# Kernel optimization log

Measured on AMD Instinct MI355X. Metric: run time of the kernel, lower is better.

The kernel has to match this reference:

```python
import jax, jax.numpy as jnp
import numpy as np

B, N, D, H = 16, 1025, 512, 8
LN_EPS = 1e-5


def _make_mask(key, n):
    # sparse adjacency over n-1 prototypes, extended with cls token (row/col 0 all ones)
    n_proto = n - 1
    adj = jax.random.bernoulli(key, 0.03, (n_proto, n_proto)).astype(jnp.float32)
    adj = jnp.clip(adj + adj.T + jnp.eye(n_proto, dtype=jnp.float32), 0.0, 1.0)
    mask = jnp.zeros((n, n), dtype=jnp.float32)
    mask = mask.at[0, :].set(1.0).at[:, 0].set(1.0)
    mask = mask.at[1:, 1:].set(adj)
    return mask


def setup_inputs() -> dict:
    key = jax.random.key(0)
    ks = jax.random.split(key, 7)
    s = 1.0 / np.sqrt(D)
    return {
        "x": jax.random.normal(ks[0], (B, N, D), dtype=jnp.float32),
        "w_qkv": jax.random.uniform(ks[1], (D, 3 * D), dtype=jnp.float32, minval=-s, maxval=s),
        "w_proj": jax.random.uniform(ks[2], (D, D), dtype=jnp.float32, minval=-s, maxval=s),
        "b_proj": jnp.zeros((D,), dtype=jnp.float32),
        "ln_gamma": jnp.ones((D,), dtype=jnp.float32),
        "ln_beta": jnp.zeros((D,), dtype=jnp.float32),
        "attn_mask": _make_mask(ks[3], N),
    }


def reference(x, w_qkv, w_proj, b_proj, ln_gamma, ln_beta, attn_mask):
    b, n, d = x.shape
    hd = d // H
    scale = hd ** -0.5
    # qkv projection: [B,N,3D] -> q,k,v each [B,H,N,hd]
    qkv = (x @ w_qkv).reshape(b, n, 3, H, hd).transpose(2, 0, 3, 1, 4)
    q, k, v = qkv[0], qkv[1], qkv[2]
    attn = jnp.einsum("bhnd,bhmd->bhnm", q, k) * scale
    attn = jnp.where(attn_mask[None, None] == 0, -jnp.inf, attn)
    attn = jax.nn.softmax(attn, axis=-1)
    o = jnp.einsum("bhnm,bhmd->bhnd", attn, v).transpose(0, 2, 1, 3).reshape(b, n, d)
    o = o @ w_proj + b_proj
    # residual: proj output + LayerNorm(proj output)
    mu = jnp.mean(o, axis=-1, keepdims=True)
    var = jnp.mean(jnp.square(o - mu), axis=-1, keepdims=True)
    ln = (o - mu) * jax.lax.rsqrt(var + LN_EPS) * ln_gamma + ln_beta
    return o + ln
```

## Files before the change

### kernel.cpp

```cpp
#include <hip/hip_runtime.h>
#include <stdint.h>

#define B_ 16
#define N_ 1025
#define D_ 512
#define H_ 8
#define HD 64
#define NP 1152
#define WM 36
#define M_ (B_*N_)
#define MP (B_*NP)
#define NTKV 17
#define NQG 72

typedef unsigned short u16;
typedef __attribute__((ext_vector_type(8))) short bf16x8;
typedef __attribute__((ext_vector_type(4))) u16 u16x4;
typedef __attribute__((ext_vector_type(8))) u16 u16x8;
typedef __attribute__((ext_vector_type(4))) float f32x4;

typedef __attribute__((address_space(1))) const uint32_t gld_t;
typedef __attribute__((address_space(3))) uint32_t lds_t;

__device__ __forceinline__ u16 f2bf(float f) {
  uint32_t u = __float_as_uint(f);
  u += 0x7FFFu + ((u >> 16) & 1u);
  return (u16)(u >> 16);
}

__device__ __forceinline__ float bf2f(u16 v) {
  return __uint_as_float(((uint32_t)v) << 16);
}

__device__ __forceinline__ uint32_t cvtpk(float a, float b) {
  uint32_t r;
  asm("v_cvt_pk_bf16_f32 %0, %1, %2" : "=v"(r) : "v"(a), "v"(b));
  return r;
}

__device__ __forceinline__ float exp2a(float x) {
  float r;
  asm("v_exp_f32 %0, %1\n\ts_nop 0" : "=v"(r) : "v"(x));
  return r;
}

__device__ __forceinline__ void gload16(const void* g, void* l) {
  __builtin_amdgcn_global_load_lds((gld_t*)g, (lds_t*)l, 16, 0, 0);
}

__global__ void k_bitmask(const float* __restrict__ mask, uint32_t* __restrict__ bm) {
  int r = blockIdx.x;
  int wave = threadIdx.x >> 6, lane = threadIdx.x & 63;
  for (int chunk = wave; chunk < 18; chunk += 4) {
    int kv = chunk * 64 + lane;
    bool pred = (r < N_) && (kv < N_) && (mask[(size_t)r * N_ + kv] != 0.0f);
    unsigned long long bal = __ballot(pred);
    if (lane == 0) {
      bm[r * WM + chunk * 2]     = (uint32_t)bal;
      bm[r * WM + chunk * 2 + 1] = (uint32_t)(bal >> 32);
    }
  }
}

__global__ __launch_bounds__(64) void k_amask(const uint32_t* __restrict__ bm, float* __restrict__ am) {
  int qg = blockIdx.x, ti = blockIdx.y;
  int lane = threadIdx.x;
  int lq = lane & 15, lg = lane >> 4;
  int q = qg * 16 + lq;
  size_t base = ((size_t)(qg * NTKV + ti) * 64 + lane) * 16;
#pragma unroll
  for (int f = 0; f < 4; ++f) {
    f32x4 o;
#pragma unroll
    for (int r = 0; r < 4; ++r) {
      int kv = ti * 64 + f * 16 + 4 * lg + r;
      uint32_t bit = (bm[q * WM + (kv >> 5)] >> (kv & 31)) & 1u;
      o[r] = bit ? 0.f : -30000.f;
    }
    *reinterpret_cast<f32x4*>(am + base + f * 4) = o;
  }
}

__global__ void k_wconv(const float* __restrict__ wqkv, const float* __restrict__ wproj,
                        u16* __restrict__ wtq, u16* __restrict__ wtp) {
  int idx = blockIdx.x * 256 + threadIdx.x;
  if (idx < 3 * D_ * D_) {
    int k = idx / (3 * D_), c = idx % (3 * D_);
    wtq[c * D_ + k] = f2bf(wqkv[idx]);
  }
  if (idx < D_ * D_) {
    int k = idx >> 9, c = idx & 511;
    wtp[c * D_ + k] = f2bf(wproj[idx]);
  }
}

__global__ void k_xconv(const float* __restrict__ x, u16* __restrict__ xb) {
  int i = blockIdx.x * 256 + threadIdx.x;
  int idx = i * 8;
  int pr = idx >> 9;
  int col = idx & 511;
  int b = pr / NP, n = pr - b * NP;
  u16x8 o;
  if (n < N_) {
    const float* src = x + ((size_t)b * N_ + n) * D_ + col;
    float4 v0 = *reinterpret_cast<const float4*>(src);
    float4 v1 = *reinterpret_cast<const float4*>(src + 4);
    o[0] = f2bf(v0.x); o[1] = f2bf(v0.y); o[2] = f2bf(v0.z); o[3] = f2bf(v0.w);
    o[4] = f2bf(v1.x); o[5] = f2bf(v1.y); o[6] = f2bf(v1.z); o[7] = f2bf(v1.w);
  } else {
    o = (u16x8){0,0,0,0,0,0,0,0};
  }
  *reinterpret_cast<u16x8*>(xb + idx) = o;
}

__global__ __launch_bounds__(256) void k_qkv(const u16* __restrict__ xb, const u16* __restrict__ wtq,
                                             u16* __restrict__ Q, u16* __restrict__ K,
                                             u16* __restrict__ Vt) {
  __shared__ u16 sA[2][128 * 64];
  __shared__ u16 sB[2][128 * 64];
  const int bid = blockIdx.x;
  const int wg = (bid & 7) * 216 + (bid >> 3);
  const int m0 = (wg / 12) * 128;
  const int n0 = (wg % 12) * 128;
  const int t = threadIdx.x;
  const int wave = t >> 6, lane = t & 63;
  const int wm = wave >> 1, wn = wave & 1;
  const int lq = lane & 15, lg = lane >> 4;

  const int srow = lane >> 3;
  const int schunk = (lane & 7) ^ srow;

  f32x4 acc[4][4] = {};

#define QSTAGE(buf, k0_)                                                          \
  {                                                                               \
    _Pragma("unroll")                                                             \
    for (int p = 0; p < 4; ++p) {                                                 \
      int row = p * 32 + wave * 8 + srow;                                         \
      gload16(xb + (size_t)(m0 + row) * 512 + (k0_) + schunk * 8,                 \
              &sA[buf][p * 2048 + wave * 512 + lane * 8]);                        \
      gload16(wtq + (size_t)(n0 + row) * 512 + (k0_) + schunk * 8,                \
              &sB[buf][p * 2048 + wave * 512 + lane * 8]);                        \
    }                                                                             \
  }

#define QCOMPUTE(buf)                                                             \
  {                                                                               \
    _Pragma("unroll")                                                             \
    for (int kk = 0; kk < 2; ++kk) {                                              \
      bf16x8 af[4], bff[4];                                                       \
      const int pc = (kk * 4 + lg) ^ (lq & 7);                                    \
      _Pragma("unroll")                                                           \
      for (int f = 0; f < 4; ++f) {                                               \
        af[f]  = *reinterpret_cast<const bf16x8*>(&sA[buf][(wm * 64 + f * 16 + lq) * 64 + pc * 8]); \
        bff[f] = *reinterpret_cast<const bf16x8*>(&sB[buf][(wn * 64 + f * 16 + lq) * 64 + pc * 8]); \
      }                                                                           \
      _Pragma("unroll")                                                           \
      for (int i = 0; i < 4; ++i)                                                 \
        _Pragma("unroll")                                                         \
        for (int j = 0; j < 4; ++j)                                               \
          acc[i][j] = __builtin_amdgcn_mfma_f32_16x16x32_bf16(af[i], bff[j], acc[i][j], 0, 0, 0); \
    }                                                                             \
  }

  QSTAGE(0, 0);
  int cur = 0;
  for (int k0 = 0; k0 < 448; k0 += 64) {
    QSTAGE(cur ^ 1, k0 + 64);
    asm volatile("s_waitcnt vmcnt(8)" ::: "memory");
    __builtin_amdgcn_s_barrier();
    QCOMPUTE(cur);
    __builtin_amdgcn_s_barrier();
    cur ^= 1;
  }
  asm volatile("s_waitcnt vmcnt(0)" ::: "memory");
  __builtin_amdgcn_s_barrier();
  QCOMPUTE(cur);
#undef QSTAGE
#undef QCOMPUTE

  if (n0 >= 1024) {
    __syncthreads();
    u16* T = (u16*)&sA[0][0];
#pragma unroll
    for (int j = 0; j < 4; ++j) {
      int c = wn * 64 + j * 16 + lq;
#pragma unroll
      for (int i = 0; i < 4; ++i) {
        int mb = wm * 64 + i * 16 + lg * 4;
        u16x4 pw;
#pragma unroll
        for (int r = 0; r < 4; ++r) pw[r] = f2bf(acc[i][j][r]);
        *reinterpret_cast<u16x4*>(&T[c * 128 + ((((mb >> 3) ^ lq) << 3) | (mb & 7))]) = pw;
      }
    }
    __syncthreads();
    int c = t & 127;
    int ch0 = (t >> 7) << 3;
    int cg = n0 + c - 1024;
    int h = cg >> 6, d = cg & 63;
    int bb = m0 / NP;
    int nb = m0 - bb * NP;
    u16* dst = Vt + (((size_t)(bb * H_ + h) * HD + d) * NP + nb);
#pragma unroll
    for (int rep = 0; rep < 8; ++rep) {
      int chunk = ch0 + rep;
      u16x8 vv = *reinterpret_cast<const u16x8*>(&T[c * 128 + ((chunk ^ (c & 15)) << 3)]);
      *reinterpret_cast<u16x8*>(&dst[chunk * 8]) = vv;
    }
  } else {
#pragma unroll
    for (int j = 0; j < 4; ++j) {
      int c = n0 + wn * 64 + j * 16 + lq;
      int which = c >> 9, h = (c >> 6) & 7, d = c & 63;
#pragma unroll
      for (int i = 0; i < 4; ++i) {
        int mbase = m0 + wm * 64 + i * 16 + lg * 4;
#pragma unroll
        for (int r = 0; r < 4; ++r) {
          int m = mbase + r;
          int b = m / NP, n = m - b * NP;
          int bh = b * H_ + h;
          float v = acc[i][j][r];
          if (which == 0) Q[((size_t)bh * NP + n) * HD + d] = f2bf(v * 0.18033688f);
          else            K[((size_t)bh * NP + n) * HD + d] = f2bf(v);
        }
      }
    }
  }
}

__global__ __launch_bounds__(512) void k_attn(const u16* __restrict__ Q, const u16* __restrict__ K,
                                              const u16* __restrict__ Vt, const float* __restrict__ am,
                                              u16* __restrict__ O) {
  __shared__ u16 sK[2][64 * 64];
  __shared__ u16 sV[2][64 * 64];
  __shared__ u16 sP[8][16 * 64];

  int bid = blockIdx.x;
  int wg = (bid & 7) * (9 * 128 / 8) + (bid >> 3);
  int bh = wg / 9, qt = wg - bh * 9;
  int b = bh >> 3, h = bh & 7;
  int t = threadIdx.x;
  int w = t >> 6, lane = t & 63;
  int lq = lane & 15, lg = lane >> 4;
  int qbase = qt * 128 + w * 16;
  int qg = qt * 8 + w;
  const u16* Qp = Q + ((size_t)bh * NP + qbase) * HD;
  const u16* Kp = K + (size_t)bh * NP * HD;
  const u16* Vp = Vt + (size_t)bh * HD * NP;
  const float* amp = am + ((size_t)qg * NTKV * 64 + lane) * 16;

  bf16x8 qf0 = *reinterpret_cast<const bf16x8*>(Qp + lq * HD + lg * 8);
  bf16x8 qf1 = *reinterpret_cast<const bf16x8*>(Qp + lq * HD + 32 + lg * 8);

  const int srow = t >> 3, sch = (t & 7) ^ (srow & 7);

  f32x4 oacc[4] = {};
  float lpart = 0.f;

#define STAGE(buf, kv0_)                                                        \
  {                                                                             \
    gload16(Kp + (size_t)((kv0_) + srow) * HD + sch * 8, &sK[buf][t * 8]);      \
    gload16(Vp + (size_t)srow * NP + (kv0_) + sch * 8,   &sV[buf][t * 8]);      \
  }

#define AML(an, ti_)                                                            \
  {                                                                             \
    const f32x4* ap = reinterpret_cast<const f32x4*>(amp + (size_t)(ti_) * 64 * 16); \
    an[0] = ap[0]; an[1] = ap[1]; an[2] = ap[2]; an[3] = ap[3];                 \
  }

#define COMPUTE(buf, ac)                                                         \
  {                                                                              \
    f32x4 s[4] = {ac[0], ac[1], ac[2], ac[3]};       \
    __builtin_amdgcn_s_setprio(1);                                               \
    _Pragma("unroll")                                                            \
    for (int kk = 0; kk < 2; ++kk) {                                             \
      bf16x8 qf = kk ? qf1 : qf0;                                                \
      int pc = (kk * 4 + lg) ^ (lq & 7);                                         \
      _Pragma("unroll")                                                          \
      for (int f = 0; f < 4; ++f) {                                              \
        bf16x8 kf = *reinterpret_cast<const bf16x8*>(&sK[buf][(f * 16 + lq) * 64 + pc * 8]); \
        s[f] = __builtin_amdgcn_mfma_f32_16x16x32_bf16(kf, qf, s[f], 0, 0, 0);   \
      }                                                                          \
    }                                                                            \
    __builtin_amdgcn_s_setprio(0);                                               \
    _Pragma("unroll")                                                            \
    for (int f = 0; f < 4; ++f) {                                                \
      _Pragma("unroll")                                                          \
      for (int r = 0; r < 4; ++r) {                                              \
        float pv = exp2a(s[f][r]);                                               \
        s[f][r] = pv;                                                            \
        lpart += pv;                                                             \
      }                                                                          \
    }                                                                            \
    _Pragma("unroll")                                                            \
    for (int f = 0; f < 4; ++f) {                                                \
      uint2 pw;                                                                  \
      pw.x = cvtpk(s[f][0], s[f][1]);                                            \
      pw.y = cvtpk(s[f][2], s[f][3]);                                            \
      int pch = (2 * f + (lg >> 1)) ^ (lq & 7);                                  \
      *reinterpret_cast<uint2*>(&sP[w][lq * 64 + pch * 8 + (lg & 1) * 4]) = pw;  \
    }                                                                            \
    __builtin_amdgcn_s_setprio(1);                                               \
    _Pragma("unroll")                                                            \
    for (int kk = 0; kk < 2; ++kk) {                                             \
      int pc = (kk * 4 + lg) ^ (lq & 7);                                         \
      bf16x8 pf = *reinterpret_cast<const bf16x8*>(&sP[w][lq * 64 + pc * 8]);    \
      _Pragma("unroll")                                                          \
      for (int j = 0; j < 4; ++j) {                                              \
        bf16x8 vf = *reinterpret_cast<const bf16x8*>(&sV[buf][(j * 16 + lq) * 64 + pc * 8]); \
        oacc[j] = __builtin_amdgcn_mfma_f32_16x16x32_bf16(pf, vf, oacc[j], 0, 0, 0); \
      }                                                                          \
    }                                                                            \
    __builtin_amdgcn_s_setprio(0);                                               \
  }

#define STEP(bufb, ac, an, ti_)                                                  \
  {                                                                              \
    STAGE((bufb) ^ 1, ((ti_) + 1) * 64);                                         \
    AML(an, (ti_) + 1);                                                          \
    asm volatile("s_waitcnt vmcnt(6)" ::: "memory");                             \
    __builtin_amdgcn_s_barrier();                                                \
    COMPUTE(bufb, ac);                                                           \
    __builtin_amdgcn_s_barrier();                                                \
  }

  f32x4 a0[4], a1[4];
  STAGE(0, 0);
  AML(a0, 0);
  for (int tp = 0; tp < 8; ++tp) {
    STEP(0, a0, a1, 2 * tp);
    STEP(1, a1, a0, 2 * tp + 1);
  }
  asm volatile("s_waitcnt vmcnt(0)" ::: "memory");
  __builtin_amdgcn_s_barrier();
  COMPUTE(0, a0);
#undef STAGE
#undef AML
#undef COMPUTE
#undef STEP

  lpart += __shfl_xor(lpart, 16);
  lpart += __shfl_xor(lpart, 32);

#pragma unroll
  for (int r = 0; r < 4; ++r) {
    int n = qbase + 4 * lg + r;
    float lr = __shfl(lpart, 4 * lg + r);
    float linv = (lr > 0.f) ? 1.f / lr : 0.f;
    size_t mrow = (size_t)b * NP + n;
#pragma unroll
    for (int j = 0; j < 4; ++j)
      O[mrow * D_ + h * HD + j * 16 + lq] = f2bf(oacc[j][r] * linv);
  }
}

__global__ __launch_bounds__(256) void k_proj(const u16* __restrict__ ob, const u16* __restrict__ wtp,
                                              const float* __restrict__ bias, u16* __restrict__ opb) {
  __shared__ u16 sA[2][128 * 64];
  __shared__ u16 sB[2][128 * 64];
  const int bid = blockIdx.x;
  const int wg = (bid & 7) * 72 + (bid >> 3);
  const int m0 = (wg >> 2) * 128;
  const int n0 = (wg & 3) * 128;
  const int t = threadIdx.x;
  const int wave = t >> 6, lane = t & 63;
  const int wm = wave >> 1, wn = wave & 1;
  const int lq = lane & 15, lg = lane >> 4;

  const int srow = lane >> 3;
  const int schunk = (lane & 7) ^ srow;

  f32x4 acc[4][4] = {};

#define PSTAGE(buf, k0_)                                                          \
  {                                                                               \
    _Pragma("unroll")                                                             \
    for (int p = 0; p < 4; ++p) {                                                 \
      int row = p * 32 + wave * 8 + srow;                                         \
      gload16(ob + (size_t)(m0 + row) * 512 + (k0_) + schunk * 8,                 \
              &sA[buf][p * 2048 + wave * 512 + lane * 8]);                        \
      gload16(wtp + (size_t)(n0 + row) * 512 + (k0_) + schunk * 8,                \
              &sB[buf][p * 2048 + wave * 512 + lane * 8]);                        \
    }                                                                             \
  }

#define PCOMPUTE(buf)                                                             \
  {                                                                               \
    _Pragma("unroll")                                                             \
    for (int kk = 0; kk < 2; ++kk) {                                              \
      bf16x8 af[4], bff[4];                                                       \
      const int pc = (kk * 4 + lg) ^ (lq & 7);                                    \
      _Pragma("unroll")                                                           \
      for (int f = 0; f < 4; ++f) {                                               \
        af[f]  = *reinterpret_cast<const bf16x8*>(&sA[buf][(wm * 64 + f * 16 + lq) * 64 + pc * 8]); \
        bff[f] = *reinterpret_cast<const bf16x8*>(&sB[buf][(wn * 64 + f * 16 + lq) * 64 + pc * 8]); \
      }                                                                           \
      _Pragma("unroll")                                                           \
      for (int i = 0; i < 4; ++i)                                                 \
        _Pragma("unroll")                                                         \
        for (int j = 0; j < 4; ++j)                                               \
          acc[i][j] = __builtin_amdgcn_mfma_f32_16x16x32_bf16(af[i], bff[j], acc[i][j], 0, 0, 0); \
    }                                                                             \
  }

  PSTAGE(0, 0);
  int cur = 0;
  for (int k0 = 0; k0 < 448; k0 += 64) {
    PSTAGE(cur ^ 1, k0 + 64);
    asm volatile("s_waitcnt vmcnt(8)" ::: "memory");
    __builtin_amdgcn_s_barrier();
    PCOMPUTE(cur);
    __builtin_amdgcn_s_barrier();
    cur ^= 1;
  }
  asm volatile("s_waitcnt vmcnt(0)" ::: "memory");
  __builtin_amdgcn_s_barrier();
  PCOMPUTE(cur);
#undef PSTAGE
#undef PCOMPUTE

#pragma unroll
  for (int j = 0; j < 4; ++j) {
    int c = n0 + wn * 64 + j * 16 + lq;
    float bv = bias[c];
#pragma unroll
    for (int i = 0; i < 4; ++i) {
      int mbase = m0 + wm * 64 + i * 16 + lg * 4;
#pragma unroll
      for (int r = 0; r < 4; ++r) {
        int m = mbase + r;
        opb[(size_t)m * D_ + c] = f2bf(acc[i][j][r] + bv);
      }
    }
  }
}

__global__ __launch_bounds__(256) void k_ln(const u16* __restrict__ opb, const float* __restrict__ gamma,
                                            const float* __restrict__ beta, float* __restrict__ out) {
  int wave = threadIdx.x >> 6, lane = threadIdx.x & 63;
  int row = blockIdx.x * 4 + wave;
  int b = row / N_, n = row - b * N_;
  const u16* src = opb + ((size_t)b * NP + n) * D_ + lane * 8;
  u16x8 ov = *reinterpret_cast<const u16x8*>(src);
  float v[8];
  float s = 0.f, sq = 0.f;
#pragma unroll
  for (int j = 0; j < 8; ++j) {
    v[j] = bf2f((u16)ov[j]);
    s += v[j];
    sq += v[j] * v[j];
  }
#pragma unroll
  for (int off = 1; off < 64; off <<= 1) { s += __shfl_xor(s, off); sq += __shfl_xor(sq, off); }
  float mu = s * (1.f / 512.f);
  float var = sq * (1.f / 512.f) - mu * mu;
  float rinv = rsqrtf(var + 1e-5f);
  float4 g0 = *reinterpret_cast<const float4*>(gamma + lane * 8);
  float4 g1 = *reinterpret_cast<const float4*>(gamma + lane * 8 + 4);
  float4 b0 = *reinterpret_cast<const float4*>(beta + lane * 8);
  float4 b1 = *reinterpret_cast<const float4*>(beta + lane * 8 + 4);
  float g[8] = {g0.x, g0.y, g0.z, g0.w, g1.x, g1.y, g1.z, g1.w};
  float bb[8] = {b0.x, b0.y, b0.z, b0.w, b1.x, b1.y, b1.z, b1.w};
  float* dst = out + (size_t)row * D_ + lane * 8;
  float4 o0, o1;
  o0.x = v[0] + (v[0] - mu) * rinv * g[0] + bb[0];
  o0.y = v[1] + (v[1] - mu) * rinv * g[1] + bb[1];
  o0.z = v[2] + (v[2] - mu) * rinv * g[2] + bb[2];
  o0.w = v[3] + (v[3] - mu) * rinv * g[3] + bb[3];
  o1.x = v[4] + (v[4] - mu) * rinv * g[4] + bb[4];
  o1.y = v[5] + (v[5] - mu) * rinv * g[5] + bb[5];
  o1.z = v[6] + (v[6] - mu) * rinv * g[6] + bb[6];
  o1.w = v[7] + (v[7] - mu) * rinv * g[7] + bb[7];
  *reinterpret_cast<float4*>(dst)     = o0;
  *reinterpret_cast<float4*>(dst + 4) = o1;
}

extern "C" void kernel_launch(void* const* d_in, const int* in_sizes, int n_in,
                              void* d_out, int out_size, void* d_ws, size_t ws_size,
                              hipStream_t stream) {
  const float* x     = (const float*)d_in[0];
  const float* wqkv  = (const float*)d_in[1];
  const float* wproj = (const float*)d_in[2];
  const float* bproj = (const float*)d_in[3];
  const float* gamma = (const float*)d_in[4];
  const float* beta  = (const float*)d_in[5];
  const float* mask  = (const float*)d_in[6];
  float* out = (float*)d_out;

  char* ws = (char*)d_ws;
  size_t off = 0;
  auto alloc = [&](size_t bytes) {
    void* p = ws + off;
    off = (off + bytes + 255) & ~(size_t)255;
    return p;
  };
  uint32_t* bmask = (uint32_t*)alloc((size_t)NP * WM * 4);
  float* am  = (float*)alloc((size_t)NQG * NTKV * 64 * 16 * 4);
  u16* wtq  = (u16*)alloc((size_t)3 * D_ * D_ * 2);
  u16* wtp  = (u16*)alloc((size_t)D_ * D_ * 2);
  u16* xb   = (u16*)alloc((size_t)MP * D_ * 2);
  u16* Qb   = (u16*)alloc((size_t)128 * NP * HD * 2);
  u16* Kb   = (u16*)alloc((size_t)128 * NP * HD * 2);
  u16* Vtb  = (u16*)alloc((size_t)128 * HD * NP * 2);
  u16* Ob   = (u16*)alloc((size_t)MP * D_ * 2);
  u16* opb  = (u16*)alloc((size_t)MP * D_ * 2);

  k_bitmask<<<dim3(NP), dim3(256), 0, stream>>>(mask, bmask);
  k_amask<<<dim3(NQG, NTKV), dim3(64), 0, stream>>>(bmask, am);
  k_wconv<<<dim3(3072), dim3(256), 0, stream>>>(wqkv, wproj, wtq, wtp);
  k_xconv<<<dim3(MP * D_ / (256 * 8)), dim3(256), 0, stream>>>(x, xb);
  k_qkv<<<dim3(12 * (MP / 128)), dim3(256), 0, stream>>>(xb, wtq, Qb, Kb, Vtb);
  k_attn<<<dim3(9 * 128), dim3(512), 0, stream>>>(Qb, Kb, Vtb, am, Ob);
  k_proj<<<dim3(4 * (MP / 128)), dim3(256), 0, stream>>>(Ob, wtp, bproj, opb);
  k_ln<<<dim3(M_ / 4), dim3(256), 0, stream>>>(opb, gamma, beta, out);
}
```

Baseline: 175.0 us.

## Drop bitmask pass, tile weight transpose via LDS, interleave P writes with PV MFMAs

Removes the separate bitmask kernel so the additive mask is built directly from the float mask, saving one launch and one intermediate buffer. The weight conversion now transposes 64x64 tiles through shared memory with coalesced reads and vectorized bf16 writes, replacing scattered per-element transposed stores. In attention, the P tile is written to and read from LDS in two 32-wide halves per kk step, which halves sP and lets the PV MFMAs for the first half begin before the second half is stored. The direct mask reads are strided per lane and less coalesced than the ballot approach.

```diff
diff --git a/kernel.cpp b/kernel.cpp
--- a/kernel.cpp
+++ b/kernel.cpp
@@ -7,7 +7,6 @@
 #define H_ 8
 #define HD 64
 #define NP 1152
-#define WM 36
 #define M_ (B_*N_)
 #define MP (B_*NP)
 #define NTKV 17
@@ -48,49 +47,65 @@
   __builtin_amdgcn_global_load_lds((gld_t*)g, (lds_t*)l, 16, 0, 0);
 }
 
-__global__ void k_bitmask(const float* __restrict__ mask, uint32_t* __restrict__ bm) {
-  int r = blockIdx.x;
-  int wave = threadIdx.x >> 6, lane = threadIdx.x & 63;
-  for (int chunk = wave; chunk < 18; chunk += 4) {
-    int kv = chunk * 64 + lane;
-    bool pred = (r < N_) && (kv < N_) && (mask[(size_t)r * N_ + kv] != 0.0f);
-    unsigned long long bal = __ballot(pred);
-    if (lane == 0) {
-      bm[r * WM + chunk * 2]     = (uint32_t)bal;
-      bm[r * WM + chunk * 2 + 1] = (uint32_t)(bal >> 32);
-    }
-  }
-}
-
-__global__ __launch_bounds__(64) void k_amask(const uint32_t* __restrict__ bm, float* __restrict__ am) {
+__global__ __launch_bounds__(64) void k_amask(const float* __restrict__ mask, float* __restrict__ am) {
   int qg = blockIdx.x, ti = blockIdx.y;
   int lane = threadIdx.x;
   int lq = lane & 15, lg = lane >> 4;
   int q = qg * 16 + lq;
   size_t base = ((size_t)(qg * NTKV + ti) * 64 + lane) * 16;
+  const float* mrow = mask + (size_t)q * N_;
+  bool qok = (q < N_);
 #pragma unroll
   for (int f = 0; f < 4; ++f) {
     f32x4 o;
+    int kvb = ti * 64 + f * 16 + 4 * lg;
 #pragma unroll
     for (int r = 0; r < 4; ++r) {
-      int kv = ti * 64 + f * 16 + 4 * lg + r;
-      uint32_t bit = (bm[q * WM + (kv >> 5)] >> (kv & 31)) & 1u;
-      o[r] = bit ? 0.f : -30000.f;
+      int kv = kvb + r;
+      bool ok = qok && (kv < N_) && (mrow[kv] != 0.0f);
+      o[r] = ok ? 0.f : -30000.f;
     }
     *reinterpret_cast<f32x4*>(am + base + f * 4) = o;
   }
 }
 
-__global__ void k_wconv(const float* __restrict__ wqkv, const float* __restrict__ wproj,
-                        u16* __restrict__ wtq, u16* __restrict__ wtp) {
-  int idx = blockIdx.x * 256 + threadIdx.x;
-  if (idx < 3 * D_ * D_) {
-    int k = idx / (3 * D_), c = idx % (3 * D_);
-    wtq[c * D_ + k] = f2bf(wqkv[idx]);
-  }
-  if (idx < D_ * D_) {
-    int k = idx >> 9, c = idx & 511;
-    wtp[c * D_ + k] = f2bf(wproj[idx]);
+__global__ __launch_bounds__(256) void k_wconv(const float* __restrict__ wqkv, const float* __restrict__ wproj,
+                                               u16* __restrict__ wtq, u16* __restrict__ wtp) {
+  __shared__ float T[64][65];
+  int bid = blockIdx.x;
+  const float* src;
+  u16* dst;
+  int sstride;
+  if (bid < 192) {
+    int kt = bid / 24, ct = bid - kt * 24;
+    src = wqkv + (size_t)(kt * 64) * 1536 + ct * 64;
+    dst = wtq + (size_t)(ct * 64) * 512 + kt * 64;
+    sstride = 1536;
+  } else {
+    int b2 = bid - 192;
+    int kt = b2 >> 3, ct = b2 & 7;
+    src = wproj + (size_t)(kt * 64) * 512 + ct * 64;
+    dst = wtp + (size_t)(ct * 64) * 512 + kt * 64;
+    sstride = 512;
+  }
+  int t = threadIdx.x;
+  int r = t >> 2, cc = (t & 3) * 16;
+#pragma unroll
+  for (int i = 0; i < 4; ++i) {
+    float4 v = *reinterpret_cast<const float4*>(src + (size_t)r * sstride + cc + i * 4);
+    T[cc + i * 4 + 0][r] = v.x;
+    T[cc + i * 4 + 1][r] = v.y;
+    T[cc + i * 4 + 2][r] = v.z;
+    T[cc + i * 4 + 3][r] = v.w;
+  }
+  __syncthreads();
+  int c = t >> 2, k0 = (t & 3) * 16;
+#pragma unroll
+  for (int rep = 0; rep < 2; ++rep) {
+    u16x8 o;
+#pragma unroll
+    for (int j = 0; j < 8; ++j) o[j] = f2bf(T[c][k0 + rep * 8 + j]);
+    *reinterpret_cast<u16x8*>(dst + (size_t)c * 512 + k0 + rep * 8) = o;
   }
 }
 
@@ -235,7 +250,7 @@
                                               u16* __restrict__ O) {
   __shared__ u16 sK[2][64 * 64];
   __shared__ u16 sV[2][64 * 64];
-  __shared__ u16 sP[8][16 * 64];
+  __shared__ u16 sP[8][16 * 32];
 
   int bid = blockIdx.x;
   int wg = (bid & 7) * (9 * 128 / 8) + (bid >> 3);
@@ -296,25 +311,27 @@
       }                                                                          \
     }                                                                            \
     _Pragma("unroll")                                                            \
-    for (int f = 0; f < 4; ++f) {                                                \
-      uint2 pw;                                                                  \
-      pw.x = cvtpk(s[f][0], s[f][1]);                                            \
-      pw.y = cvtpk(s[f][2], s[f][3]);                                            \
-      int pch = (2 * f + (lg >> 1)) ^ (lq & 7);                                  \
-      *reinterpret_cast<uint2*>(&sP[w][lq * 64 + pch * 8 + (lg & 1) * 4]) = pw;  \
-    }                                                                            \
-    __builtin_amdgcn_s_setprio(1);                                               \
-    _Pragma("unroll")                                                            \
     for (int kk = 0; kk < 2; ++kk) {                                             \
-      int pc = (kk * 4 + lg) ^ (lq & 7);                                         \
-      bf16x8 pf = *reinterpret_cast<const bf16x8*>(&sP[w][lq * 64 + pc * 8]);    \
+      _Pragma("unroll")                                                          \
+      for (int fi = 0; fi < 2; ++fi) {                                           \
+        int f = kk * 2 + fi;                                                     \
+        uint2 pw;                                                                \
+        pw.x = cvtpk(s[f][0], s[f][1]);                                          \
+        pw.y = cvtpk(s[f][2], s[f][3]);                                          \
+        int pch2 = (2 * fi + (lg >> 1)) ^ (lq & 3);                              \
+        *reinterpret_cast<uint2*>(&sP[w][lq * 32 + pch2 * 8 + (lg & 1) * 4]) = pw; \
+      }                                                                          \
+      int pc2 = lg ^ (lq & 3);                                                   \
+      int pcv = (kk * 4 + lg) ^ (lq & 7);                                        \
+      bf16x8 pf = *reinterpret_cast<const bf16x8*>(&sP[w][lq * 32 + pc2 * 8]);   \
+      __builtin_amdgcn_s_setprio(1);                                             \
       _Pragma("unroll")                                                          \
       for (int j = 0; j < 4; ++j) {                                              \
-        bf16x8 vf = *reinterpret_cast<const bf16x8*>(&sV[buf][(j * 16 + lq) * 64 + pc * 8]); \
+        bf16x8 vf = *reinterpret_cast<const bf16x8*>(&sV[buf][(j * 16 + lq) * 64 + pcv * 8]); \
         oacc[j] = __builtin_amdgcn_mfma_f32_16x16x32_bf16(pf, vf, oacc[j], 0, 0, 0); \
       }                                                                          \
+      __builtin_amdgcn_s_setprio(0);                                             \
     }                                                                            \
-    __builtin_amdgcn_s_setprio(0);                                               \
   }
 
 #define STEP(bufb, ac, an, ti_)                                                  \
@@ -497,8 +514,7 @@
     off = (off + bytes + 255) & ~(size_t)255;
     return p;
   };
-  uint32_t* bmask = (uint32_t*)alloc((size_t)NP * WM * 4);
-  float* am  = (float*)alloc((size_t)NQG * NTKV * 64 * 16 * 4);
+  float* am = (float*)alloc((size_t)NQG * NTKV * 64 * 16 * 4);
   u16* wtq  = (u16*)alloc((size_t)3 * D_ * D_ * 2);
   u16* wtp  = (u16*)alloc((size_t)D_ * D_ * 2);
   u16* xb   = (u16*)alloc((size_t)MP * D_ * 2);
@@ -508,9 +524,8 @@
   u16* Ob   = (u16*)alloc((size_t)MP * D_ * 2);
   u16* opb  = (u16*)alloc((size_t)MP * D_ * 2);
 
-  k_bitmask<<<dim3(NP), dim3(256), 0, stream>>>(mask, bmask);
-  k_amask<<<dim3(NQG, NTKV), dim3(64), 0, stream>>>(bmask, am);
-  k_wconv<<<dim3(3072), dim3(256), 0, stream>>>(wqkv, wproj, wtq, wtp);
+  k_amask<<<dim3(NQG, NTKV), dim3(64), 0, stream>>>(mask, am);
+  k_wconv<<<dim3(256), dim3(256), 0, stream>>>(wqkv, wproj, wtq, wtp);
   k_xconv<<<dim3(MP * D_ / (256 * 8)), dim3(256), 0, stream>>>(x, xb);
   k_qkv<<<dim3(12 * (MP / 128)), dim3(256), 0, stream>>>(xb, wtq, Qb, Kb, Vtb);
   k_attn<<<dim3(9 * 128), dim3(512), 0, stream>>>(Qb, Kb, Vtb, am, Ob);
```

Result: faster. 169.9 us (-3.0%).
